# Kernel optimization log

Hardware: AMD Instinct MI355X
Metric: run time of the kernel (lower is better)

Reference implementation:

```python
import jax, jax.numpy as jnp
import numpy as np

N, E, B, L, D, H = 50000, 800000, 64, 32, 256, 256


def setup_inputs() -> dict:
    key = jax.random.key(0)
    ks = jax.random.split(key, 20)
    s = 0.05
    inp = {
        'x': jax.random.normal(ks[0], (N, D), jnp.float32),
        'edge_index': jax.random.randint(ks[1], (2, E), 0, N),
        'batch': jnp.sort(jax.random.randint(ks[2], (N,), 0, B)),
        'paths': jax.random.randint(ks[3], (B, L), 0, N),
        # SAGEConv1: lin_l (aggregated neighbors, with bias) + lin_r (root, no bias)
        'w1l': jax.random.normal(ks[4], (D, H), jnp.float32) * s,
        'b1l': jnp.zeros((H,), jnp.float32),
        'w1r': jax.random.normal(ks[5], (D, H), jnp.float32) * s,
        # SAGEConv2
        'w2l': jax.random.normal(ks[6], (H, H), jnp.float32) * s,
        'b2l': jnp.zeros((H,), jnp.float32),
        'w2r': jax.random.normal(ks[7], (H, H), jnp.float32) * s,
        # LSTM (gate order i,f,g,o as in torch)
        'w_ih': jax.random.normal(ks[8], (4 * H, H), jnp.float32) * s,
        'w_hh': jax.random.normal(ks[9], (4 * H, H), jnp.float32) * s,
        'b_ih': jnp.zeros((4 * H,), jnp.float32),
        'b_hh': jnp.zeros((4 * H,), jnp.float32),
        # scorer MLP
        'wm1': jax.random.normal(ks[10], (2 * H, H), jnp.float32) * s,
        'bm1': jnp.zeros((H,), jnp.float32),
        'wm2': jax.random.normal(ks[11], (H, 1), jnp.float32) * s,
        'bm2': jnp.zeros((1,), jnp.float32),
    }
    return inp


def sage_conv(x, src, dst, wl, bl, wr):
    # mean-aggregate neighbor features (messages flow src -> dst)
    agg = jax.ops.segment_sum(x[src], dst, num_segments=N)
    deg = jax.ops.segment_sum(jnp.ones((src.shape[0],), x.dtype), dst, num_segments=N)
    mean = agg / jnp.maximum(deg, 1.0)[:, None]
    return mean @ wl + bl + x @ wr


def lstm_last_hidden(seq, w_ih, w_hh, b_ih, b_hh):
    # seq: [B, L, H] -> hn: [B, H]
    h0 = jnp.zeros((seq.shape[0], H), seq.dtype)
    c0 = jnp.zeros_like(h0)

    def step(carry, xt):
        h, c = carry
        gates = xt @ w_ih.T + b_ih + h @ w_hh.T + b_hh
        i, f, g, o = jnp.split(gates, 4, axis=-1)
        c = jax.nn.sigmoid(f) * c + jax.nn.sigmoid(i) * jnp.tanh(g)
        h = jax.nn.sigmoid(o) * jnp.tanh(c)
        return (h, c), None

    (hn, _), _ = jax.lax.scan(step, (h0, c0), jnp.swapaxes(seq, 0, 1))
    return hn


def reference(x, edge_index, batch, paths, w1l, b1l, w1r, w2l, b2l, w2r,
              w_ih, w_hh, b_ih, b_hh, wm1, bm1, wm2, bm2):
    src, dst = edge_index[0], edge_index[1]
    h = jax.nn.relu(sage_conv(x, src, dst, w1l, b1l, w1r))
    node_emb = sage_conv(h, src, dst, w2l, b2l, w2r)  # [N, H]

    # global mean pool per graph
    gsum = jax.ops.segment_sum(node_emb, batch, num_segments=B)
    gcnt = jax.ops.segment_sum(jnp.ones((N,), node_emb.dtype), batch, num_segments=B)
    graph_emb = gsum / jnp.maximum(gcnt, 1.0)[:, None]  # [B, H]

    path_seq = node_emb[paths]  # [B, L, H]
    path_emb = lstm_last_hidden(path_seq, w_ih, w_hh, b_ih, b_hh)  # [B, H]

    combined = jnp.concatenate([graph_emb, path_emb], axis=-1)  # [B, 2H]
    scores = jax.nn.relu(combined @ wm1 + bm1) @ wm2 + bm2  # [B, 1]
    return scores.reshape(-1)  # torch.cat of per-path [1] scores -> [B]
```

## Files before the change

kernel.cpp:

```cpp
#include <hip/hip_runtime.h>

namespace {

constexpr int NN = 50000;
constexpr int NE = 800000;
constexpr int NB = 64;
constexpr int NL = 32;
constexpr int ND = 256;
constexpr int NSCAN = 196;
constexpr int NPOOL = (NN + 63) / 64;

typedef __attribute__((ext_vector_type(8))) short short8v;
typedef __attribute__((ext_vector_type(4))) float float4v;

#define GLD16(GP, LP) __builtin_amdgcn_global_load_lds( \
    (const __attribute__((address_space(1))) void*)(GP), \
    (__attribute__((address_space(3))) void*)(LP), 16, 0, 0)

__device__ __forceinline__ float sigf(float x){ return 1.0f/(1.0f + __expf(-x)); }

__device__ __forceinline__ ushort rne_bf16(float f){
  uint u = __float_as_uint(f);
  return (ushort)((u + 0x7FFFu + ((u >> 16) & 1u)) >> 16);
}
__device__ __forceinline__ float bf2f(ushort u){ return __uint_as_float((uint)u << 16); }

__device__ __forceinline__ void split1(float f, ushort& h, ushort& lo){
  uint u = __float_as_uint(f);
  h = (ushort)(u >> 16);
  float r = f - __uint_as_float(u & 0xFFFF0000u);
  lo = (ushort)(__float_as_uint(r) >> 16);
}

__device__ __forceinline__ void split8(float4 fa, float4 fb, uint4& h, uint4& lo){
  uint a0=__float_as_uint(fa.x), a1=__float_as_uint(fa.y), a2=__float_as_uint(fa.z), a3=__float_as_uint(fa.w);
  uint b0=__float_as_uint(fb.x), b1=__float_as_uint(fb.y), b2=__float_as_uint(fb.z), b3=__float_as_uint(fb.w);
  h.x = (a0>>16) | (a1 & 0xFFFF0000u);
  h.y = (a2>>16) | (a3 & 0xFFFF0000u);
  h.z = (b0>>16) | (b1 & 0xFFFF0000u);
  h.w = (b2>>16) | (b3 & 0xFFFF0000u);
  float r0 = fa.x - __uint_as_float(a0 & 0xFFFF0000u);
  float r1 = fa.y - __uint_as_float(a1 & 0xFFFF0000u);
  float r2 = fa.z - __uint_as_float(a2 & 0xFFFF0000u);
  float r3 = fa.w - __uint_as_float(a3 & 0xFFFF0000u);
  float r4 = fb.x - __uint_as_float(b0 & 0xFFFF0000u);
  float r5 = fb.y - __uint_as_float(b1 & 0xFFFF0000u);
  float r6 = fb.z - __uint_as_float(b2 & 0xFFFF0000u);
  float r7 = fb.w - __uint_as_float(b3 & 0xFFFF0000u);
  lo.x = (__float_as_uint(r0)>>16) | (__float_as_uint(r1) & 0xFFFF0000u);
  lo.y = (__float_as_uint(r2)>>16) | (__float_as_uint(r3) & 0xFFFF0000u);
  lo.z = (__float_as_uint(r4)>>16) | (__float_as_uint(r5) & 0xFFFF0000u);
  lo.w = (__float_as_uint(r6)>>16) | (__float_as_uint(r7) & 0xFFFF0000u);
}

__global__ void k_hist(const int* __restrict__ dst, int* __restrict__ cnt){
  int stride = gridDim.x * blockDim.x;
  for (int e = blockIdx.x*blockDim.x + threadIdx.x; e < NE; e += stride)
    atomicAdd(&cnt[dst[e]], 1);
}

__global__ void k_scan_block(const int* __restrict__ cnt, int* __restrict__ offs,
                             int* __restrict__ bsum){
  __shared__ int s[256];
  const int t = threadIdx.x, i = blockIdx.x*256 + t;
  int v = cnt[i];
  s[t] = v; __syncthreads();
  #pragma unroll
  for (int off = 1; off < 256; off <<= 1){
    int x = (t >= off) ? s[t-off] : 0;
    __syncthreads();
    s[t] += x;
    __syncthreads();
  }
  offs[i] = s[t] - v;
  if (t == 255) bsum[blockIdx.x] = s[255];
}

__global__ void k_scan_top(const int* __restrict__ bsum, int* __restrict__ bsum2){
  __shared__ int s[256];
  const int t = threadIdx.x;
  int v = (t < NSCAN) ? bsum[t] : 0;
  s[t] = v; __syncthreads();
  #pragma unroll
  for (int off = 1; off < 256; off <<= 1){
    int x = (t >= off) ? s[t-off] : 0;
    __syncthreads();
    s[t] += x;
    __syncthreads();
  }
  if (t < NSCAN) bsum2[t] = s[t] - v;
}

__global__ void k_scan_add(int* __restrict__ offs, const int* __restrict__ bsum2,
                           int* __restrict__ cursor){
  const int i = blockIdx.x*256 + threadIdx.x;
  int v = offs[i] + bsum2[blockIdx.x];
  offs[i] = v;
  cursor[i] = v;
}

__global__ void k_fill(const int* __restrict__ src, const int* __restrict__ dst,
                       int* __restrict__ cursor, int* __restrict__ csr){
  int stride = gridDim.x * blockDim.x;
  for (int e = blockIdx.x*blockDim.x + threadIdx.x; e < NE; e += stride){
    int d = dst[e];
    int pos = atomicAdd(&cursor[d], 1);
    csr[pos] = src[e];
  }
}

__global__ void k_tobf16(const float* __restrict__ in, ushort* __restrict__ out){
  const int i = blockIdx.x*blockDim.x + threadIdx.x;
  const float4 a = ((const float4*)in)[i*2];
  const float4 b = ((const float4*)in)[i*2+1];
  ushort o[8] = { rne_bf16(a.x), rne_bf16(a.y), rne_bf16(a.z), rne_bf16(a.w),
                  rne_bf16(b.x), rne_bf16(b.y), rne_bf16(b.z), rne_bf16(b.w) };
  ((uint4*)out)[i] = *(uint4*)o;
}

__launch_bounds__(256, 8)
__global__ void k_gather_bf16(const ushort* __restrict__ feat, const int* __restrict__ offs,
                              const int* __restrict__ csr,
                              ushort* __restrict__ outH, ushort* __restrict__ outL){
  __shared__ float4 sp[256];
  const int u = blockIdx.x, t = threadIdx.x;
  const int w = t >> 6, l = t & 63;
  const int beg = offs[u], end = offs[u+1];
  const int lc = l * 4;
  float a0 = 0.f, a1 = 0.f, a2 = 0.f, a3 = 0.f;
  int e = beg + w;
  for (; e + 4 < end; e += 8){
    int s0 = csr[e], s1 = csr[e+4];
    ushort4 v0 = *(const ushort4*)(feat + (long long)s0*ND + lc);
    ushort4 v1 = *(const ushort4*)(feat + (long long)s1*ND + lc);
    a0 += bf2f(v0.x) + bf2f(v1.x);
    a1 += bf2f(v0.y) + bf2f(v1.y);
    a2 += bf2f(v0.z) + bf2f(v1.z);
    a3 += bf2f(v0.w) + bf2f(v1.w);
  }
  if (e < end){
    int s0 = csr[e];
    ushort4 v0 = *(const ushort4*)(feat + (long long)s0*ND + lc);
    a0 += bf2f(v0.x); a1 += bf2f(v0.y); a2 += bf2f(v0.z); a3 += bf2f(v0.w);
  }
  sp[t] = make_float4(a0, a1, a2, a3);
  __syncthreads();
  if (t < 64){
    float4 p0 = sp[t], p1 = sp[64+t], p2 = sp[128+t], p3 = sp[192+t];
    float inv = 1.0f / fmaxf((float)(end - beg), 1.0f);
    float4 r;
    r.x = (p0.x + p1.x + p2.x + p3.x) * inv;
    r.y = (p0.y + p1.y + p2.y + p3.y) * inv;
    r.z = (p0.z + p1.z + p2.z + p3.z) * inv;
    r.w = (p0.w + p1.w + p2.w + p3.w) * inv;
    ushort hh[4], ll[4];
    split1(r.x, hh[0], ll[0]);
    split1(r.y, hh[1], ll[1]);
    split1(r.z, hh[2], ll[2]);
    split1(r.w, hh[3], ll[3]);
    *(ushort4*)(outH + (long long)u*ND + t*4) = *(ushort4*)hh;
    *(ushort4*)(outL + (long long)u*ND + t*4) = *(ushort4*)ll;
  }
}

__global__ void k_wsplit(const float* __restrict__ wl, const float* __restrict__ wr,
                         ushort* __restrict__ WtH, ushort* __restrict__ WtL){
  const int k = blockIdx.x;
  const int n = threadIdx.x;
  float v = (k < 256) ? wl[k*256 + n] : wr[(k-256)*256 + n];
  uint u = __float_as_uint(v);
  float r = v - __uint_as_float(u & 0xFFFF0000u);
  const int wc = n >> 6, nt = (n >> 4) & 3, lm = n & 15;
  const int kk = k >> 5, lq = (k >> 3) & 3, j = k & 7;
  const long long idx = (long long)(((wc*4 + nt)*16 + kk)*64 + lq*16 + lm)*8 + j;
  WtH[idx] = (ushort)(u >> 16);
  WtL[idx] = (ushort)(__float_as_uint(r) >> 16);
}

__launch_bounds__(256, 3)
__global__ void k_gemm_mfma(const ushort* __restrict__ A1H, const ushort* __restrict__ A1L,
                            const ushort* __restrict__ A2H, const ushort* __restrict__ A2L,
                            const float* __restrict__ A2F,
                            const ushort* __restrict__ WtH, const ushort* __restrict__ WtL,
                            const float* __restrict__ bias,
                            ushort* __restrict__ CH, ushort* __restrict__ CL,
                            ushort* __restrict__ Cb, int relu, int a2f32)
{
  __shared__ float eb[16*260];
  char* const sm = (char*)eb;

  const int t  = threadIdx.x;
  const int w  = t >> 6;
  const int l  = t & 63;
  const int lm = l & 15;
  const int lq = l >> 4;
  const int m0 = blockIdx.x * 64;

  const uint4* BH4 = (const uint4*)WtH;
  const uint4* BL4 = (const uint4*)WtL;

  const float4v vzero = {0.f, 0.f, 0.f, 0.f};
  float4v acc[4][4];
  #pragma unroll
  for (int i = 0; i < 4; ++i)
    #pragma unroll
    for (int j = 0; j < 4; ++j) acc[i][j] = vzero;

  int bbase[4];
  #pragma unroll
  for (int nt = 0; nt < 4; ++nt) bbase[nt] = (w*4 + nt)*1024 + l;

  const int j0 = w * 2;

  auto stageHL = [&](int bb, const ushort* __restrict__ H, const ushort* __restrict__ L, int k0){
    #pragma unroll
    for (int jj = 0; jj < 2; ++jj){
      const int j   = j0 + jj;
      const int arr = j >> 2;
      const int i   = j & 3;
      const int row = i*16 + (l >> 2);
      int rg = m0 + row; rg = (rg < NN) ? rg : (NN - 1);
      const int g = (l & 3) ^ ((row >> 1) & 3);
      const ushort* srcp = (arr ? L : H) + (long long)rg*ND + k0 + g*8;
      GLD16(srcp, sm + bb + arr*4096 + i*1024);
    }
  };
  auto stageF = [&](int bb, int k0){
    #pragma unroll
    for (int jj = 0; jj < 2; ++jj){
      const int j   = j0 + jj;
      const int row = j*8 + (l >> 3);
      int rg = m0 + row; rg = (rg < NN) ? rg : (NN - 1);
      const int g = (l & 7) ^ (row & 7);
      const float* srcp = A2F + (long long)rg*ND + k0 + g*4;
      GLD16(srcp, sm + bb + j*1024);
    }
  };
  auto stage = [&](int bb, int kk){
    if (kk < 8)      stageHL(bb, A1H, A1L, kk*32);
    else if (!a2f32) stageHL(bb, A2H, A2L, (kk - 8)*32);
    else             stageF (bb, (kk - 8)*32);
  };

  stage(0, 0);
  __syncthreads();

  #pragma unroll
  for (int kk = 0; kk < 16; ++kk){
    const int bb = (kk & 1) * 8192;

    uint4 bh[4], bl[4];
    #pragma unroll
    for (int nt = 0; nt < 4; ++nt){
      const int idx = bbase[nt] + kk*64;
      bh[nt] = BH4[idx];
      bl[nt] = BL4[idx];
    }

    if (kk < 15) stage(bb ^ 8192, kk + 1);

    uint4 ah[4], al[4];
    if (kk < 8 || !a2f32){
      #pragma unroll
      for (int mt = 0; mt < 4; ++mt){
        const int row = mt*16 + lm;
        const int off = bb + row*64 + ((lq ^ ((row >> 1) & 3)) << 4);
        ah[mt] = *(const uint4*)(sm + off);
        al[mt] = *(const uint4*)(sm + 4096 + off);
      }
    } else {
      #pragma unroll
      for (int mt = 0; mt < 4; ++mt){
        const int row = mt*16 + lm;
        const int s = row & 7;
        const float4 fa = *(const float4*)(sm + bb + row*128 + (((2*lq    ) ^ s) << 4));
        const float4 fb = *(const float4*)(sm + bb + row*128 + (((2*lq + 1) ^ s) << 4));
        split8(fa, fb, ah[mt], al[mt]);
      }
    }

    #pragma unroll
    for (int nt = 0; nt < 4; ++nt){
      short8v bhv = *(short8v*)&bh[nt];
      short8v blv = *(short8v*)&bl[nt];
      #pragma unroll
      for (int mt = 0; mt < 4; ++mt){
        short8v ahv = *(short8v*)&ah[mt];
        short8v alv = *(short8v*)&al[mt];
        acc[mt][nt] = __builtin_amdgcn_mfma_f32_16x16x32_bf16(ahv, bhv, acc[mt][nt], 0, 0, 0);
        acc[mt][nt] = __builtin_amdgcn_mfma_f32_16x16x32_bf16(alv, bhv, acc[mt][nt], 0, 0, 0);
        acc[mt][nt] = __builtin_amdgcn_mfma_f32_16x16x32_bf16(ahv, blv, acc[mt][nt], 0, 0, 0);
      }
    }
    __syncthreads();
  }

  float bvv[4];
  #pragma unroll
  for (int nt = 0; nt < 4; ++nt) bvv[nt] = bias[w*64 + nt*16 + lm];

  #pragma unroll
  for (int mt = 0; mt < 4; ++mt){
    #pragma unroll
    for (int nt = 0; nt < 4; ++nt){
      #pragma unroll
      for (int r = 0; r < 4; ++r){
        float v = acc[mt][nt][r] + bvv[nt];
        if (relu) v = fmaxf(v, 0.f);
        eb[(lq*4 + r)*260 + w*64 + nt*16 + lm] = v;
      }
    }
    __syncthreads();
    #pragma unroll
    for (int i = 0; i < 4; ++i){
      int idx = i*256 + t;
      int rr  = idx >> 6;
      int c4  = (idx & 63) * 4;
      int grow = m0 + mt*16 + rr;
      if (grow < NN){
        float4 fv = *(float4*)&eb[rr*260 + c4];
        ushort hh[4], ll[4];
        split1(fv.x, hh[0], ll[0]);
        split1(fv.y, hh[1], ll[1]);
        split1(fv.z, hh[2], ll[2]);
        split1(fv.w, hh[3], ll[3]);
        *(ushort4*)(CH + (long long)grow*ND + c4) = *(ushort4*)hh;
        *(ushort4*)(CL + (long long)grow*ND + c4) = *(ushort4*)ll;
        if (Cb){
          ushort ub[4] = { rne_bf16(fv.x), rne_bf16(fv.y), rne_bf16(fv.z), rne_bf16(fv.w) };
          *(ushort4*)(Cb + (long long)grow*ND + c4) = *(ushort4*)ub;
        }
      }
    }
    __syncthreads();
  }
}

__launch_bounds__(256, 3)
__global__ void k_xgate(const ushort* __restrict__ EH, const ushort* __restrict__ EL,
                        const int* __restrict__ paths,
                        const float* __restrict__ w_ih, const float* __restrict__ b_ih,
                        const float* __restrict__ b_hh, float* __restrict__ xg)
{
  __shared__ float As[16][68];
  __shared__ float Ws[16][260];
  const int t  = threadIdx.x;
  const int m0 = blockIdx.x * 64;
  const int g0 = blockIdx.y * 256;
  const int rg = t >> 5, cg = t & 31;
  const int sm = t >> 2, sj = (t & 3) * 4;

  float acc[8][8];
  #pragma unroll
  for (int i = 0; i < 8; ++i)
    #pragma unroll
    for (int j = 0; j < 8; ++j) acc[i][j] = 0.f;

  const int node = paths[m0 + sm];
  const ushort* ehrow = EH + (long long)node*ND;
  const ushort* elrow = EL + (long long)node*ND;
  const float* wrow = w_ih + (long long)(g0 + t)*ND;

  for (int k0 = 0; k0 < 256; k0 += 16){
    ushort4 hv = *(const ushort4*)(ehrow + k0 + sj);
    ushort4 lv = *(const ushort4*)(elrow + k0 + sj);
    float av0 = bf2f(hv.x) + bf2f(lv.x);
    float av1 = bf2f(hv.y) + bf2f(lv.y);
    float av2 = bf2f(hv.z) + bf2f(lv.z);
    float av3 = bf2f(hv.w) + bf2f(lv.w);
    float4 q0 = *(const float4*)(wrow + k0 + 0);
    float4 q1 = *(const float4*)(wrow + k0 + 4);
    float4 q2 = *(const float4*)(wrow + k0 + 8);
    float4 q3 = *(const float4*)(wrow + k0 + 12);
    __syncthreads();
    As[sj+0][sm]=av0; As[sj+1][sm]=av1; As[sj+2][sm]=av2; As[sj+3][sm]=av3;
    Ws[ 0][t]=q0.x; Ws[ 1][t]=q0.y; Ws[ 2][t]=q0.z; Ws[ 3][t]=q0.w;
    Ws[ 4][t]=q1.x; Ws[ 5][t]=q1.y; Ws[ 6][t]=q1.z; Ws[ 7][t]=q1.w;
    Ws[ 8][t]=q2.x; Ws[ 9][t]=q2.y; Ws[10][t]=q2.z; Ws[11][t]=q2.w;
    Ws[12][t]=q3.x; Ws[13][t]=q3.y; Ws[14][t]=q3.z; Ws[15][t]=q3.w;
    __syncthreads();
    #pragma unroll
    for (int k = 0; k < 16; ++k){
      float a[8], b[8];
      *(float4*)&a[0] = *(const float4*)&As[k][rg*8];
      *(float4*)&a[4] = *(const float4*)&As[k][rg*8+4];
      *(float4*)&b[0] = *(const float4*)&Ws[k][cg*8];
      *(float4*)&b[4] = *(const float4*)&Ws[k][cg*8+4];
      #pragma unroll
      for (int i = 0; i < 8; ++i)
        #pragma unroll
        for (int j = 0; j < 8; ++j)
          acc[i][j] = fmaf(a[i], b[j], acc[i][j]);
    }
  }

  float bv[8];
  #pragma unroll
  for (int j = 0; j < 8; ++j){ int g = g0 + cg*8 + j; bv[j] = b_ih[g] + b_hh[g]; }
  #pragma unroll
  for (int i = 0; i < 8; ++i){
    int row = m0 + rg*8 + i;
    float o[8];
    #pragma unroll
    for (int j = 0; j < 8; ++j) o[j] = acc[i][j] + bv[j];
    *(float4*)(xg + (long long)row*1024 + g0 + cg*8 + 0) = *(float4*)&o[0];
    *(float4*)(xg + (long long)row*1024 + g0 + cg*8 + 4) = *(float4*)&o[4];
  }
}

__launch_bounds__(256, 4)
__global__ void k_lstm_step(const float* __restrict__ h_in, float* __restrict__ h_out,
                            float* __restrict__ c_state, const float* __restrict__ xg,
                            const float* __restrict__ w_hh, int tstep)
{
  __shared__ float ws[4*256];
  __shared__ float hs[32*260];
  __shared__ float part[2*128];
  __shared__ float gs[128];
  const int t  = threadIdx.x;
  const int u  = blockIdx.x >> 1;
  const int b0 = (blockIdx.x & 1) * 32;

  {
    int gate = t >> 6, c4 = (t & 63) * 4;
    float4 v = *(const float4*)(w_hh + (long long)(gate*256 + u)*256 + c4);
    *(float4*)&ws[gate*256 + c4] = v;
  }
  #pragma unroll
  for (int i = 0; i < 8; ++i){
    int idx = i*256 + t;
    int b = idx >> 6, c4 = (idx & 63) * 4;
    float4 v = *(const float4*)(h_in + (long long)(b0 + b)*256 + c4);
    *(float4*)&hs[b*260 + c4] = v;
  }
  __syncthreads();

  const int b  = t & 31;
  const int g  = (t >> 5) & 3;
  const int kd = t >> 7;
  float s = 0.f;
  const float* hp = &hs[b*260 + kd*128];
  const float* wp = &ws[g*256 + kd*128];
  #pragma unroll
  for (int k4 = 0; k4 < 32; ++k4){
    float4 h4 = *(const float4*)(hp + k4*4);
    float4 w4 = *(const float4*)(wp + k4*4);
    s += h4.x*w4.x + h4.y*w4.y + h4.z*w4.z + h4.w*w4.w;
  }
  part[kd*128 + b*4 + g] = s;
  __syncthreads();

  if (t < 128){
    int bb = t >> 2, gg = t & 3;
    const float* xp = xg + ((long long)(b0 + bb)*NL + tstep)*1024;
    gs[t] = part[t] + part[128 + t] + xp[gg*256 + u];
  }
  __syncthreads();

  if (t < 32){
    float gi = gs[t*4+0], gf = gs[t*4+1], gG = gs[t*4+2], go = gs[t*4+3];
    int bb = b0 + t;
    float c_old = c_state[bb*256 + u];
    float c_new = sigf(gf)*c_old + sigf(gi)*tanhf(gG);
    c_state[bb*256 + u] = c_new;
    h_out[bb*256 + u] = sigf(go)*tanhf(c_new);
  }
}

__launch_bounds__(256, 8)
__global__ void k_pool(const ushort* __restrict__ EH, const ushort* __restrict__ EL,
                       const int* __restrict__ batch,
                       float* __restrict__ gsum, float* __restrict__ gcnt)
{
  __shared__ int bs[64];
  __shared__ int uni;
  __shared__ float spf[8*256];
  const int t  = threadIdx.x;
  const int m0 = blockIdx.x * 64;
  const int r  = t >> 5;
  const int c  = t & 31;
  if (t == 0) uni = 1;
  if (t < 64){
    int n = m0 + t;
    bs[t] = (n < NN) ? batch[n] : -1;
  }
  __syncthreads();
  if (t < 64 && bs[t] != bs[0]) uni = 0;
  __syncthreads();

  const ushort* eh = EH + (long long)m0*ND + c*8;
  const ushort* el = EL + (long long)m0*ND + c*8;

  if (uni){
    float a[8];
    #pragma unroll
    for (int j = 0; j < 8; ++j) a[j] = 0.f;
    #pragma unroll
    for (int i = 0; i < 8; ++i){
      const int row = r*8 + i;
      const uint4 hv = *(const uint4*)(eh + (long long)row*ND);
      const uint4 lv = *(const uint4*)(el + (long long)row*ND);
      const ushort* hp = (const ushort*)&hv;
      const ushort* lp = (const ushort*)&lv;
      #pragma unroll
      for (int j = 0; j < 8; ++j) a[j] += bf2f(hp[j]) + bf2f(lp[j]);
    }
    #pragma unroll
    for (int j = 0; j < 8; ++j) spf[r*256 + c*8 + j] = a[j];
    __syncthreads();
    float s = spf[t] + spf[256+t] + spf[512+t] + spf[768+t]
            + spf[1024+t] + spf[1280+t] + spf[1536+t] + spf[1792+t];
    const int g = bs[0];
    unsafeAtomicAdd(&gsum[g*256 + t], s);
    if (t == 0) unsafeAtomicAdd(&gcnt[g], 64.0f);
  } else {
    float a[8];
    #pragma unroll
    for (int j = 0; j < 8; ++j) a[j] = 0.f;
    int cur = -1, cnt = 0;
    #pragma unroll
    for (int i = 0; i < 8; ++i){
      const int row = r*8 + i;
      const int g = bs[row];
      if (g != cur){
        if (cur >= 0){
          #pragma unroll
          for (int j = 0; j < 8; ++j) unsafeAtomicAdd(&gsum[cur*256 + c*8 + j], a[j]);
          if (c == 0) unsafeAtomicAdd(&gcnt[cur], (float)cnt);
        }
        #pragma unroll
        for (int j = 0; j < 8; ++j) a[j] = 0.f;
        cnt = 0; cur = g;
      }
      if (g >= 0){
        const uint4 hv = *(const uint4*)(eh + (long long)row*ND);
        const uint4 lv = *(const uint4*)(el + (long long)row*ND);
        const ushort* hp = (const ushort*)&hv;
        const ushort* lp = (const ushort*)&lv;
        #pragma unroll
        for (int j = 0; j < 8; ++j) a[j] += bf2f(hp[j]) + bf2f(lp[j]);
        ++cnt;
      }
    }
    if (cur >= 0){
      #pragma unroll
      for (int j = 0; j < 8; ++j) unsafeAtomicAdd(&gsum[cur*256 + c*8 + j], a[j]);
      if (c == 0) unsafeAtomicAdd(&gcnt[cur], (float)cnt);
    }
  }
}

__global__ void k_score(const float* __restrict__ gsum, const float* __restrict__ gcnt,
                        const float* __restrict__ hfin, const float* __restrict__ wm1,
                        const float* __restrict__ bm1, const float* __restrict__ wm2,
                        const float* __restrict__ bm2, float* __restrict__ out)
{
  __shared__ float cs[512];
  __shared__ float red[4];
  const int b = blockIdx.x, t = threadIdx.x;
  float inv = 1.0f / fmaxf(gcnt[b], 1.0f);
  cs[t]       = gsum[b*256 + t] * inv;
  cs[256 + t] = hfin[b*256 + t];
  __syncthreads();
  float v = 0.f;
  #pragma unroll 4
  for (int k = 0; k < 512; ++k) v = fmaf(cs[k], wm1[(long long)k*256 + t], v);
  v = fmaxf(v + bm1[t], 0.f) * wm2[t];
  #pragma unroll
  for (int off = 32; off > 0; off >>= 1) v += __shfl_down(v, off, 64);
  if ((t & 63) == 0) red[t >> 6] = v;
  __syncthreads();
  if (t == 0) out[b] = red[0] + red[1] + red[2] + red[3] + bm2[0];
}

}

extern "C" void kernel_launch(void* const* d_in, const int* in_sizes, int n_in,
                              void* d_out, int out_size, void* d_ws, size_t ws_size,
                              hipStream_t stream)
{
  const float* x     = (const float*)d_in[0];
  const int*   eidx  = (const int*)  d_in[1];
  const int*   batch = (const int*)  d_in[2];
  const int*   paths = (const int*)  d_in[3];
  const float* w1l   = (const float*)d_in[4];
  const float* b1l   = (const float*)d_in[5];
  const float* w1r   = (const float*)d_in[6];
  const float* w2l   = (const float*)d_in[7];
  const float* b2l   = (const float*)d_in[8];
  const float* w2r   = (const float*)d_in[9];
  const float* w_ih  = (const float*)d_in[10];
  const float* w_hh  = (const float*)d_in[11];
  const float* b_ih  = (const float*)d_in[12];
  const float* b_hh  = (const float*)d_in[13];
  const float* wm1   = (const float*)d_in[14];
  const float* bm1   = (const float*)d_in[15];
  const float* wm2   = (const float*)d_in[16];
  const float* bm2   = (const float*)d_in[17];

  const int* src = eidx;
  const int* dst = eidx + NE;

  float* w    = (float*)d_ws;
  float* bufA = w;
  float* bufB = bufA + (long long)NN*ND;
  float* xg   = bufB + (long long)NN*ND;
  float* gsum = xg   + 2048*1024;
  float* gcnt = gsum + NB*ND;
  float* h0   = gcnt + 64;
  float* c0   = h0   + NB*ND;
  float* h1   = c0   + NB*ND;
  ushort* wt1H = (ushort*)(h1 + NB*ND);
  ushort* wt1L = wt1H + 256*512;
  ushort* wt2H = wt1L + 256*512;
  ushort* wt2L = wt2H + 256*512;
  ushort* fb16 = wt2L + 256*512;

  ushort* A1H = (ushort*)bufA;
  ushort* A1L = A1H + (long long)NN*ND;
  ushort* h1H = (ushort*)bufB;
  ushort* h1L = h1H + (long long)NN*ND;

  int* cnt    = (int*)xg;
  int* offs   = cnt    + 50432;
  int* cursor = offs   + 50432;
  int* bsum   = cursor + 50432;
  int* bsum2  = bsum   + 256;
  int* csr    = bsum2  + 256;

  k_wsplit<<<512, 256, 0, stream>>>(w1l, w1r, wt1H, wt1L);
  k_wsplit<<<512, 256, 0, stream>>>(w2l, w2r, wt2H, wt2L);

  k_tobf16<<<(NN*ND/8 + 255)/256, 256, 0, stream>>>(x, fb16);

  hipMemsetAsync(cnt, 0, 50432*sizeof(int), stream);
  k_hist<<<1024, 256, 0, stream>>>(dst, cnt);
  k_scan_block<<<NSCAN, 256, 0, stream>>>(cnt, offs, bsum);
  k_scan_top<<<1, 256, 0, stream>>>(bsum, bsum2);
  k_scan_add<<<NSCAN, 256, 0, stream>>>(offs, bsum2, cursor);
  k_fill<<<1024, 256, 0, stream>>>(src, dst, cursor, csr);

  k_gather_bf16<<<NN, 256, 0, stream>>>(fb16, offs, csr, A1H, A1L);
  k_gemm_mfma<<<(NN+63)/64, 256, 0, stream>>>(A1H, A1L, nullptr, nullptr, x,
                                              wt1H, wt1L, b1l, h1H, h1L, fb16, 1, 1);

  k_gather_bf16<<<NN, 256, 0, stream>>>(fb16, offs, csr, A1H, A1L);
  k_gemm_mfma<<<(NN+63)/64, 256, 0, stream>>>(A1H, A1L, h1H, h1L, nullptr,
                                              wt2H, wt2L, b2l, h1H, h1L, (ushort*)nullptr, 0, 0);

  hipMemsetAsync(gsum, 0, (NB*ND + 64)*sizeof(float), stream);
  k_pool<<<NPOOL, 256, 0, stream>>>(h1H, h1L, batch, gsum, gcnt);

  k_xgate<<<dim3((NB*NL)/64, 1024/256), 256, 0, stream>>>(h1H, h1L, paths, w_ih, b_ih, b_hh, xg);

  hipMemsetAsync(h0, 0, 2*(size_t)NB*ND*sizeof(float), stream);
  for (int ts = 0; ts < NL; ++ts){
    float* hin  = (ts & 1) ? h1 : h0;
    float* hout = (ts & 1) ? h0 : h1;
    k_lstm_step<<<512, 256, 0, stream>>>(hin, hout, c0, xg, w_hh, ts);
  }

  k_score<<<NB, 256, 0, stream>>>(gsum, gcnt, h0, wm1, bm1, wm2, bm2, (float*)d_out);
}
```

Baseline: 786.0 us.

## Split GEMM into per-layer kernels with register-prefetched A loads, drop LDS staging

The single GEMM kernel is replaced by two specialised kernels. Both drop LDS staging via global_load_lds and instead double-buffer A (and, for layer 2, B) tiles directly in registers, with no barrier in the k-loop. Layer 1 is split across two N-halves to launch more blocks, and it no longer writes a separate bf16 copy of h1. Instead, the layer-2 gather reads the hi part of the split, which is now rounded to nearest, so the extra output stream goes away. The cost is higher register pressure and uncoalesced direct global loads of A rows.

```diff
diff --git a/kernel.cpp b/kernel.cpp
--- a/kernel.cpp
+++ b/kernel.cpp
@@ -13,10 +13,6 @@
 typedef __attribute__((ext_vector_type(8))) short short8v;
 typedef __attribute__((ext_vector_type(4))) float float4v;
 
-#define GLD16(GP, LP) __builtin_amdgcn_global_load_lds( \
-    (const __attribute__((address_space(1))) void*)(GP), \
-    (__attribute__((address_space(3))) void*)(LP), 16, 0, 0)
-
 __device__ __forceinline__ float sigf(float x){ return 1.0f/(1.0f + __expf(-x)); }
 
 __device__ __forceinline__ ushort rne_bf16(float f){
@@ -25,10 +21,9 @@
 }
 __device__ __forceinline__ float bf2f(ushort u){ return __uint_as_float((uint)u << 16); }
 
-__device__ __forceinline__ void split1(float f, ushort& h, ushort& lo){
-  uint u = __float_as_uint(f);
-  h = (ushort)(u >> 16);
-  float r = f - __uint_as_float(u & 0xFFFF0000u);
+__device__ __forceinline__ void splitr(float f, ushort& h, ushort& lo){
+  h = rne_bf16(f);
+  float r = f - bf2f(h);
   lo = (ushort)(__float_as_uint(r) >> 16);
 }
 
@@ -154,10 +149,10 @@
     r.z = (p0.z + p1.z + p2.z + p3.z) * inv;
     r.w = (p0.w + p1.w + p2.w + p3.w) * inv;
     ushort hh[4], ll[4];
-    split1(r.x, hh[0], ll[0]);
-    split1(r.y, hh[1], ll[1]);
-    split1(r.z, hh[2], ll[2]);
-    split1(r.w, hh[3], ll[3]);
+    splitr(r.x, hh[0], ll[0]);
+    splitr(r.y, hh[1], ll[1]);
+    splitr(r.z, hh[2], ll[2]);
+    splitr(r.w, hh[3], ll[3]);
     *(ushort4*)(outH + (long long)u*ND + t*4) = *(ushort4*)hh;
     *(ushort4*)(outL + (long long)u*ND + t*4) = *(ushort4*)ll;
   }
@@ -178,121 +173,210 @@
 }
 
 __launch_bounds__(256, 3)
-__global__ void k_gemm_mfma(const ushort* __restrict__ A1H, const ushort* __restrict__ A1L,
-                            const ushort* __restrict__ A2H, const ushort* __restrict__ A2L,
-                            const float* __restrict__ A2F,
-                            const ushort* __restrict__ WtH, const ushort* __restrict__ WtL,
-                            const float* __restrict__ bias,
-                            ushort* __restrict__ CH, ushort* __restrict__ CL,
-                            ushort* __restrict__ Cb, int relu, int a2f32)
+__global__ void k_gemm_l1(const ushort* __restrict__ A1H, const ushort* __restrict__ A1L,
+                          const float* __restrict__ A2F,
+                          const ushort* __restrict__ WtH, const ushort* __restrict__ WtL,
+                          const float* __restrict__ bias,
+                          ushort* __restrict__ CH, ushort* __restrict__ CL)
 {
-  __shared__ float eb[16*260];
-  char* const sm = (char*)eb;
-
+  __shared__ float eb[16*132];
   const int t  = threadIdx.x;
   const int w  = t >> 6;
   const int l  = t & 63;
   const int lm = l & 15;
   const int lq = l >> 4;
   const int m0 = blockIdx.x * 64;
+  const int n0 = blockIdx.y * 128;
 
   const uint4* BH4 = (const uint4*)WtH;
   const uint4* BL4 = (const uint4*)WtL;
 
   const float4v vzero = {0.f, 0.f, 0.f, 0.f};
+  float4v acc[4][2];
+  #pragma unroll
+  for (int i = 0; i < 4; ++i)
+    #pragma unroll
+    for (int j = 0; j < 2; ++j) acc[i][j] = vzero;
+
+  long long arow[4];
+  #pragma unroll
+  for (int mt = 0; mt < 4; ++mt){
+    int row = m0 + mt*16 + lm;
+    row = (row < NN) ? row : (NN - 1);
+    arow[mt] = (long long)row * ND;
+  }
+  int bbase[2];
+  #pragma unroll
+  for (int j = 0; j < 2; ++j){
+    const int ncol = n0 + w*32 + j*16;
+    bbase[j] = ((ncol >> 6)*4 + ((ncol >> 4) & 3))*1024 + l;
+  }
+
+  auto ldA = [&](int kk, uint4* ah, uint4* al){
+    if (kk < 8){
+      const int koff = kk*32 + lq*8;
+      #pragma unroll
+      for (int mt = 0; mt < 4; ++mt){
+        ah[mt] = *(const uint4*)(A1H + arow[mt] + koff);
+        al[mt] = *(const uint4*)(A1L + arow[mt] + koff);
+      }
+    } else {
+      const int koff = (kk & 7)*32 + lq*8;
+      #pragma unroll
+      for (int mt = 0; mt < 4; ++mt){
+        const float* p = A2F + arow[mt] + koff;
+        float4 fa = *(const float4*)p;
+        float4 fb = *(const float4*)(p + 4);
+        split8(fa, fb, ah[mt], al[mt]);
+      }
+    }
+  };
+
+  uint4 ahb[2][4], alb[2][4];
+  ldA(0, ahb[0], alb[0]);
+
+  #pragma unroll
+  for (int kk = 0; kk < 16; ++kk){
+    const int cur = kk & 1, nx = cur ^ 1;
+    uint4 bh[2], bl[2];
+    #pragma unroll
+    for (int j = 0; j < 2; ++j){
+      const int idx = bbase[j] + kk*64;
+      bh[j] = BH4[idx];
+      bl[j] = BL4[idx];
+    }
+    if (kk < 15) ldA(kk + 1, ahb[nx], alb[nx]);
+
+    #pragma unroll
+    for (int j = 0; j < 2; ++j){
+      short8v bhv = *(short8v*)&bh[j];
+      short8v blv = *(short8v*)&bl[j];
+      #pragma unroll
+      for (int mt = 0; mt < 4; ++mt){
+        short8v ahv = *(short8v*)&ahb[cur][mt];
+        short8v alv = *(short8v*)&alb[cur][mt];
+        acc[mt][j] = __builtin_amdgcn_mfma_f32_16x16x32_bf16(ahv, bhv, acc[mt][j], 0, 0, 0);
+        acc[mt][j] = __builtin_amdgcn_mfma_f32_16x16x32_bf16(alv, bhv, acc[mt][j], 0, 0, 0);
+        acc[mt][j] = __builtin_amdgcn_mfma_f32_16x16x32_bf16(ahv, blv, acc[mt][j], 0, 0, 0);
+      }
+    }
+  }
+
+  float bvv[2];
+  #pragma unroll
+  for (int j = 0; j < 2; ++j) bvv[j] = bias[n0 + w*32 + j*16 + lm];
+
+  #pragma unroll
+  for (int mt = 0; mt < 4; ++mt){
+    #pragma unroll
+    for (int j = 0; j < 2; ++j){
+      #pragma unroll
+      for (int r = 0; r < 4; ++r){
+        float v = fmaxf(acc[mt][j][r] + bvv[j], 0.f);
+        eb[(lq*4 + r)*132 + w*32 + j*16 + lm] = v;
+      }
+    }
+    __syncthreads();
+    #pragma unroll
+    for (int i = 0; i < 2; ++i){
+      int idx = i*256 + t;
+      int rr  = idx >> 5;
+      int c4  = (idx & 31) * 4;
+      int grow = m0 + mt*16 + rr;
+      if (grow < NN){
+        float4 fv = *(float4*)&eb[rr*132 + c4];
+        ushort hh[4], ll[4];
+        splitr(fv.x, hh[0], ll[0]);
+        splitr(fv.y, hh[1], ll[1]);
+        splitr(fv.z, hh[2], ll[2]);
+        splitr(fv.w, hh[3], ll[3]);
+        *(ushort4*)(CH + (long long)grow*ND + n0 + c4) = *(ushort4*)hh;
+        *(ushort4*)(CL + (long long)grow*ND + n0 + c4) = *(ushort4*)ll;
+      }
+    }
+    __syncthreads();
+  }
+}
+
+__launch_bounds__(256, 2)
+__global__ void k_gemm_l2(const ushort* A1H, const ushort* A1L,
+                          const ushort* A2H, const ushort* A2L,
+                          const ushort* __restrict__ WtH, const ushort* __restrict__ WtL,
+                          const float* __restrict__ bias,
+                          ushort* CH, ushort* CL)
+{
+  __shared__ float eb[16*260];
+  const int t  = threadIdx.x;
+  const int w  = t >> 6;
+  const int l  = t & 63;
+  const int lm = l & 15;
+  const int lq = l >> 4;
+  const int m0 = blockIdx.x * 64;
+
+  const uint4* BH4 = (const uint4*)WtH;
+  const uint4* BL4 = (const uint4*)WtL;
+
+  const float4v vzero = {0.f, 0.f, 0.f, 0.f};
   float4v acc[4][4];
   #pragma unroll
   for (int i = 0; i < 4; ++i)
     #pragma unroll
     for (int j = 0; j < 4; ++j) acc[i][j] = vzero;
 
+  long long arow[4];
+  #pragma unroll
+  for (int mt = 0; mt < 4; ++mt){
+    int row = m0 + mt*16 + lm;
+    row = (row < NN) ? row : (NN - 1);
+    arow[mt] = (long long)row * ND;
+  }
   int bbase[4];
   #pragma unroll
   for (int nt = 0; nt < 4; ++nt) bbase[nt] = (w*4 + nt)*1024 + l;
 
-  const int j0 = w * 2;
-
-  auto stageHL = [&](int bb, const ushort* __restrict__ H, const ushort* __restrict__ L, int k0){
-    #pragma unroll
-    for (int jj = 0; jj < 2; ++jj){
-      const int j   = j0 + jj;
-      const int arr = j >> 2;
-      const int i   = j & 3;
-      const int row = i*16 + (l >> 2);
-      int rg = m0 + row; rg = (rg < NN) ? rg : (NN - 1);
-      const int g = (l & 3) ^ ((row >> 1) & 3);
-      const ushort* srcp = (arr ? L : H) + (long long)rg*ND + k0 + g*8;
-      GLD16(srcp, sm + bb + arr*4096 + i*1024);
-    }
-  };
-  auto stageF = [&](int bb, int k0){
-    #pragma unroll
-    for (int jj = 0; jj < 2; ++jj){
-      const int j   = j0 + jj;
-      const int row = j*8 + (l >> 3);
-      int rg = m0 + row; rg = (rg < NN) ? rg : (NN - 1);
-      const int g = (l & 7) ^ (row & 7);
-      const float* srcp = A2F + (long long)rg*ND + k0 + g*4;
-      GLD16(srcp, sm + bb + j*1024);
-    }
-  };
-  auto stage = [&](int bb, int kk){
-    if (kk < 8)      stageHL(bb, A1H, A1L, kk*32);
-    else if (!a2f32) stageHL(bb, A2H, A2L, (kk - 8)*32);
-    else             stageF (bb, (kk - 8)*32);
-  };
-
-  stage(0, 0);
-  __syncthreads();
-
-  #pragma unroll
-  for (int kk = 0; kk < 16; ++kk){
-    const int bb = (kk & 1) * 8192;
-
-    uint4 bh[4], bl[4];
+  auto ldB = [&](int kk, uint4* bh, uint4* bl){
     #pragma unroll
     for (int nt = 0; nt < 4; ++nt){
       const int idx = bbase[nt] + kk*64;
       bh[nt] = BH4[idx];
       bl[nt] = BL4[idx];
     }
-
-    if (kk < 15) stage(bb ^ 8192, kk + 1);
-
-    uint4 ah[4], al[4];
-    if (kk < 8 || !a2f32){
+  };
+  auto ldA = [&](int kk, uint4* ah, uint4* al){
+    const ushort* Hb = (kk < 8) ? A1H : A2H;
+    const ushort* Lb = (kk < 8) ? A1L : A2L;
+    const int koff = (kk & 7)*32 + lq*8;
+    #pragma unroll
+    for (int mt = 0; mt < 4; ++mt){
+      ah[mt] = *(const uint4*)(Hb + arow[mt] + koff);
+      al[mt] = *(const uint4*)(Lb + arow[mt] + koff);
+    }
+  };
+
+  uint4 bhb[2][4], blb[2][4], ahb[2][4], alb[2][4];
+  ldB(0, bhb[0], blb[0]);
+  ldA(0, ahb[0], alb[0]);
+
+  #pragma unroll
+  for (int kk = 0; kk < 16; ++kk){
+    const int cur = kk & 1, nx = cur ^ 1;
+    if (kk < 15){
+      ldB(kk + 1, bhb[nx], blb[nx]);
+      ldA(kk + 1, ahb[nx], alb[nx]);
+    }
+    #pragma unroll
+    for (int nt = 0; nt < 4; ++nt){
+      short8v bhv = *(short8v*)&bhb[cur][nt];
+      short8v blv = *(short8v*)&blb[cur][nt];
       #pragma unroll
       for (int mt = 0; mt < 4; ++mt){
-        const int row = mt*16 + lm;
-        const int off = bb + row*64 + ((lq ^ ((row >> 1) & 3)) << 4);
-        ah[mt] = *(const uint4*)(sm + off);
-        al[mt] = *(const uint4*)(sm + 4096 + off);
-      }
-    } else {
-      #pragma unroll
-      for (int mt = 0; mt < 4; ++mt){
-        const int row = mt*16 + lm;
-        const int s = row & 7;
-        const float4 fa = *(const float4*)(sm + bb + row*128 + (((2*lq    ) ^ s) << 4));
-        const float4 fb = *(const float4*)(sm + bb + row*128 + (((2*lq + 1) ^ s) << 4));
-        split8(fa, fb, ah[mt], al[mt]);
-      }
-    }
-
-    #pragma unroll
-    for (int nt = 0; nt < 4; ++nt){
-      short8v bhv = *(short8v*)&bh[nt];
-      short8v blv = *(short8v*)&bl[nt];
-      #pragma unroll
-      for (int mt = 0; mt < 4; ++mt){
-        short8v ahv = *(short8v*)&ah[mt];
-        short8v alv = *(short8v*)&al[mt];
+        short8v ahv = *(short8v*)&ahb[cur][mt];
+        short8v alv = *(short8v*)&alb[cur][mt];
         acc[mt][nt] = __builtin_amdgcn_mfma_f32_16x16x32_bf16(ahv, bhv, acc[mt][nt], 0, 0, 0);
         acc[mt][nt] = __builtin_amdgcn_mfma_f32_16x16x32_bf16(alv, bhv, acc[mt][nt], 0, 0, 0);
         acc[mt][nt] = __builtin_amdgcn_mfma_f32_16x16x32_bf16(ahv, blv, acc[mt][nt], 0, 0, 0);
       }
     }
-    __syncthreads();
   }
 
   float bvv[4];
@@ -306,7 +390,6 @@
       #pragma unroll
       for (int r = 0; r < 4; ++r){
         float v = acc[mt][nt][r] + bvv[nt];
-        if (relu) v = fmaxf(v, 0.f);
         eb[(lq*4 + r)*260 + w*64 + nt*16 + lm] = v;
       }
     }
@@ -320,16 +403,12 @@
       if (grow < NN){
         float4 fv = *(float4*)&eb[rr*260 + c4];
         ushort hh[4], ll[4];
-        split1(fv.x, hh[0], ll[0]);
-        split1(fv.y, hh[1], ll[1]);
-        split1(fv.z, hh[2], ll[2]);
-        split1(fv.w, hh[3], ll[3]);
+        splitr(fv.x, hh[0], ll[0]);
+        splitr(fv.y, hh[1], ll[1]);
+        splitr(fv.z, hh[2], ll[2]);
+        splitr(fv.w, hh[3], ll[3]);
         *(ushort4*)(CH + (long long)grow*ND + c4) = *(ushort4*)hh;
         *(ushort4*)(CL + (long long)grow*ND + c4) = *(ushort4*)ll;
-        if (Cb){
-          ushort ub[4] = { rne_bf16(fv.x), rne_bf16(fv.y), rne_bf16(fv.z), rne_bf16(fv.w) };
-          *(ushort4*)(Cb + (long long)grow*ND + c4) = *(ushort4*)ub;
-        }
       }
     }
     __syncthreads();
@@ -641,12 +720,10 @@
   k_fill<<<1024, 256, 0, stream>>>(src, dst, cursor, csr);
 
   k_gather_bf16<<<NN, 256, 0, stream>>>(fb16, offs, csr, A1H, A1L);
-  k_gemm_mfma<<<(NN+63)/64, 256, 0, stream>>>(A1H, A1L, nullptr, nullptr, x,
-                                              wt1H, wt1L, b1l, h1H, h1L, fb16, 1, 1);
-
-  k_gather_bf16<<<NN, 256, 0, stream>>>(fb16, offs, csr, A1H, A1L);
-  k_gemm_mfma<<<(NN+63)/64, 256, 0, stream>>>(A1H, A1L, h1H, h1L, nullptr,
-                                              wt2H, wt2L, b2l, h1H, h1L, (ushort*)nullptr, 0, 0);
+  k_gemm_l1<<<dim3(782, 2), 256, 0, stream>>>(A1H, A1L, x, wt1H, wt1L, b1l, h1H, h1L);
+
+  k_gather_bf16<<<NN, 256, 0, stream>>>(h1H, offs, csr, A1H, A1L);
+  k_gemm_l2<<<782, 256, 0, stream>>>(A1H, A1L, h1H, h1L, wt2H, wt2L, b2l, h1H, h1L);
 
   hipMemsetAsync(gsum, 0, (NB*ND + 64)*sizeof(float), stream);
   k_pool<<<NPOOL, 256, 0, stream>>>(h1H, h1L, batch, gsum, gcnt);
```

Measured after the change: 884.8 us. 12.6% more time.

## Load GEMM A tiles directly to registers with triple buffering, drop LDS staging

Applied to the files above, without the earlier changes.

The MFMA GEMM no longer stages A tiles through LDS with global_load_lds and per-iteration barriers. Each lane now loads its A fragments straight into registers with a 3-deep rotating buffer and double-buffered B loads, and the kernel is templated on the f32/relu flags. The split now rounds the high part to nearest, so that high half can feed the second-layer gather directly, which removes the separate bf16 copy write. The cost is higher register pressure (launch bounds lowered to 2 blocks) and uncoalesced direct global loads of A rows without LDS reuse.

```diff
diff --git a/kernel.cpp b/kernel.cpp
--- a/kernel.cpp
+++ b/kernel.cpp
@@ -13,10 +13,6 @@
 typedef __attribute__((ext_vector_type(8))) short short8v;
 typedef __attribute__((ext_vector_type(4))) float float4v;
 
-#define GLD16(GP, LP) __builtin_amdgcn_global_load_lds( \
-    (const __attribute__((address_space(1))) void*)(GP), \
-    (__attribute__((address_space(3))) void*)(LP), 16, 0, 0)
-
 __device__ __forceinline__ float sigf(float x){ return 1.0f/(1.0f + __expf(-x)); }
 
 __device__ __forceinline__ ushort rne_bf16(float f){
@@ -25,10 +21,9 @@
 }
 __device__ __forceinline__ float bf2f(ushort u){ return __uint_as_float((uint)u << 16); }
 
-__device__ __forceinline__ void split1(float f, ushort& h, ushort& lo){
-  uint u = __float_as_uint(f);
-  h = (ushort)(u >> 16);
-  float r = f - __uint_as_float(u & 0xFFFF0000u);
+__device__ __forceinline__ void splitr(float f, ushort& h, ushort& lo){
+  h = rne_bf16(f);
+  float r = f - bf2f(h);
   lo = (ushort)(__float_as_uint(r) >> 16);
 }
 
@@ -154,10 +149,10 @@
     r.z = (p0.z + p1.z + p2.z + p3.z) * inv;
     r.w = (p0.w + p1.w + p2.w + p3.w) * inv;
     ushort hh[4], ll[4];
-    split1(r.x, hh[0], ll[0]);
-    split1(r.y, hh[1], ll[1]);
-    split1(r.z, hh[2], ll[2]);
-    split1(r.w, hh[3], ll[3]);
+    splitr(r.x, hh[0], ll[0]);
+    splitr(r.y, hh[1], ll[1]);
+    splitr(r.z, hh[2], ll[2]);
+    splitr(r.w, hh[3], ll[3]);
     *(ushort4*)(outH + (long long)u*ND + t*4) = *(ushort4*)hh;
     *(ushort4*)(outL + (long long)u*ND + t*4) = *(ushort4*)ll;
   }
@@ -177,18 +172,16 @@
   WtL[idx] = (ushort)(__float_as_uint(r) >> 16);
 }
 
-__launch_bounds__(256, 3)
-__global__ void k_gemm_mfma(const ushort* __restrict__ A1H, const ushort* __restrict__ A1L,
-                            const ushort* __restrict__ A2H, const ushort* __restrict__ A2L,
-                            const float* __restrict__ A2F,
-                            const ushort* __restrict__ WtH, const ushort* __restrict__ WtL,
-                            const float* __restrict__ bias,
-                            ushort* __restrict__ CH, ushort* __restrict__ CL,
-                            ushort* __restrict__ Cb, int relu, int a2f32)
+template<int A2F32, int RELU>
+__launch_bounds__(256, 2)
+__global__ void k_gemm(const ushort* A1H, const ushort* A1L,
+                       const ushort* A2H, const ushort* A2L,
+                       const float*  A2F,
+                       const ushort* __restrict__ WtH, const ushort* __restrict__ WtL,
+                       const float* __restrict__ bias,
+                       ushort* CH, ushort* CL)
 {
   __shared__ float eb[16*260];
-  char* const sm = (char*)eb;
-
   const int t  = threadIdx.x;
   const int w  = t >> 6;
   const int l  = t & 63;
@@ -206,83 +199,77 @@
     #pragma unroll
     for (int j = 0; j < 4; ++j) acc[i][j] = vzero;
 
+  long long arow[4];
+  #pragma unroll
+  for (int mt = 0; mt < 4; ++mt){
+    int row = m0 + mt*16 + lm;
+    row = (row < NN) ? row : (NN - 1);
+    arow[mt] = (long long)row * ND;
+  }
   int bbase[4];
   #pragma unroll
   for (int nt = 0; nt < 4; ++nt) bbase[nt] = (w*4 + nt)*1024 + l;
 
-  const int j0 = w * 2;
-
-  auto stageHL = [&](int bb, const ushort* __restrict__ H, const ushort* __restrict__ L, int k0){
-    #pragma unroll
-    for (int jj = 0; jj < 2; ++jj){
-      const int j   = j0 + jj;
-      const int arr = j >> 2;
-      const int i   = j & 3;
-      const int row = i*16 + (l >> 2);
-      int rg = m0 + row; rg = (rg < NN) ? rg : (NN - 1);
-      const int g = (l & 3) ^ ((row >> 1) & 3);
-      const ushort* srcp = (arr ? L : H) + (long long)rg*ND + k0 + g*8;
-      GLD16(srcp, sm + bb + arr*4096 + i*1024);
-    }
-  };
-  auto stageF = [&](int bb, int k0){
-    #pragma unroll
-    for (int jj = 0; jj < 2; ++jj){
-      const int j   = j0 + jj;
-      const int row = j*8 + (l >> 3);
-      int rg = m0 + row; rg = (rg < NN) ? rg : (NN - 1);
-      const int g = (l & 7) ^ (row & 7);
-      const float* srcp = A2F + (long long)rg*ND + k0 + g*4;
-      GLD16(srcp, sm + bb + j*1024);
-    }
-  };
-  auto stage = [&](int bb, int kk){
-    if (kk < 8)      stageHL(bb, A1H, A1L, kk*32);
-    else if (!a2f32) stageHL(bb, A2H, A2L, (kk - 8)*32);
-    else             stageF (bb, (kk - 8)*32);
-  };
-
-  stage(0, 0);
-  __syncthreads();
-
-  #pragma unroll
-  for (int kk = 0; kk < 16; ++kk){
-    const int bb = (kk & 1) * 8192;
-
-    uint4 bh[4], bl[4];
+  uint4 aP[3][4], aQ[3][4];
+  uint4 bh[2][4], bl[2][4];
+
+  auto ldB = [&](int kk, int s){
     #pragma unroll
     for (int nt = 0; nt < 4; ++nt){
       const int idx = bbase[nt] + kk*64;
-      bh[nt] = BH4[idx];
-      bl[nt] = BL4[idx];
-    }
-
-    if (kk < 15) stage(bb ^ 8192, kk + 1);
+      bh[s][nt] = BH4[idx];
+      bl[s][nt] = BL4[idx];
+    }
+  };
+  auto ldA = [&](int kk, int s){
+    const int koff = (kk & 7)*32 + lq*8;
+    if (kk < 8 || !A2F32){
+      const ushort* Hb = (kk < 8) ? A1H : A2H;
+      const ushort* Lb = (kk < 8) ? A1L : A2L;
+      #pragma unroll
+      for (int mt = 0; mt < 4; ++mt){
+        aP[s][mt] = *(const uint4*)(Hb + arow[mt] + koff);
+        aQ[s][mt] = *(const uint4*)(Lb + arow[mt] + koff);
+      }
+    } else {
+      #pragma unroll
+      for (int mt = 0; mt < 4; ++mt){
+        const float* p = A2F + arow[mt] + koff;
+        aP[s][mt] = *(const uint4*)p;
+        aQ[s][mt] = *(const uint4*)(p + 4);
+      }
+    }
+  };
+
+  ldA(0, 0);
+  ldB(0, 0);
+  ldA(1, 1);
+
+  #pragma unroll
+  for (int kk = 0; kk < 16; ++kk){
+    const int c3 = kk % 3;
+    const int cB = kk & 1;
+    if (kk < 15) ldB(kk + 1, cB ^ 1);
+    if (kk < 14) ldA(kk + 2, (kk + 2) % 3);
+    __builtin_amdgcn_sched_barrier(0);
 
     uint4 ah[4], al[4];
-    if (kk < 8 || !a2f32){
+    if (kk < 8 || !A2F32){
+      #pragma unroll
+      for (int mt = 0; mt < 4; ++mt){ ah[mt] = aP[c3][mt]; al[mt] = aQ[c3][mt]; }
+    } else {
       #pragma unroll
       for (int mt = 0; mt < 4; ++mt){
-        const int row = mt*16 + lm;
-        const int off = bb + row*64 + ((lq ^ ((row >> 1) & 3)) << 4);
-        ah[mt] = *(const uint4*)(sm + off);
-        al[mt] = *(const uint4*)(sm + 4096 + off);
-      }
-    } else {
-      #pragma unroll
-      for (int mt = 0; mt < 4; ++mt){
-        const int row = mt*16 + lm;
-        const int s = row & 7;
-        const float4 fa = *(const float4*)(sm + bb + row*128 + (((2*lq    ) ^ s) << 4));
-        const float4 fb = *(const float4*)(sm + bb + row*128 + (((2*lq + 1) ^ s) << 4));
+        float4 fa = *(float4*)&aP[c3][mt];
+        float4 fb = *(float4*)&aQ[c3][mt];
         split8(fa, fb, ah[mt], al[mt]);
       }
     }
 
     #pragma unroll
     for (int nt = 0; nt < 4; ++nt){
-      short8v bhv = *(short8v*)&bh[nt];
-      short8v blv = *(short8v*)&bl[nt];
+      short8v bhv = *(short8v*)&bh[cB][nt];
+      short8v blv = *(short8v*)&bl[cB][nt];
       #pragma unroll
       for (int mt = 0; mt < 4; ++mt){
         short8v ahv = *(short8v*)&ah[mt];
@@ -292,7 +279,6 @@
         acc[mt][nt] = __builtin_amdgcn_mfma_f32_16x16x32_bf16(ahv, blv, acc[mt][nt], 0, 0, 0);
       }
     }
-    __syncthreads();
   }
 
   float bvv[4];
@@ -306,7 +292,7 @@
       #pragma unroll
       for (int r = 0; r < 4; ++r){
         float v = acc[mt][nt][r] + bvv[nt];
-        if (relu) v = fmaxf(v, 0.f);
+        if (RELU) v = fmaxf(v, 0.f);
         eb[(lq*4 + r)*260 + w*64 + nt*16 + lm] = v;
       }
     }
@@ -320,16 +306,12 @@
       if (grow < NN){
         float4 fv = *(float4*)&eb[rr*260 + c4];
         ushort hh[4], ll[4];
-        split1(fv.x, hh[0], ll[0]);
-        split1(fv.y, hh[1], ll[1]);
-        split1(fv.z, hh[2], ll[2]);
-        split1(fv.w, hh[3], ll[3]);
+        splitr(fv.x, hh[0], ll[0]);
+        splitr(fv.y, hh[1], ll[1]);
+        splitr(fv.z, hh[2], ll[2]);
+        splitr(fv.w, hh[3], ll[3]);
         *(ushort4*)(CH + (long long)grow*ND + c4) = *(ushort4*)hh;
         *(ushort4*)(CL + (long long)grow*ND + c4) = *(ushort4*)ll;
-        if (Cb){
-          ushort ub[4] = { rne_bf16(fv.x), rne_bf16(fv.y), rne_bf16(fv.z), rne_bf16(fv.w) };
-          *(ushort4*)(Cb + (long long)grow*ND + c4) = *(ushort4*)ub;
-        }
       }
     }
     __syncthreads();
@@ -641,12 +623,12 @@
   k_fill<<<1024, 256, 0, stream>>>(src, dst, cursor, csr);
 
   k_gather_bf16<<<NN, 256, 0, stream>>>(fb16, offs, csr, A1H, A1L);
-  k_gemm_mfma<<<(NN+63)/64, 256, 0, stream>>>(A1H, A1L, nullptr, nullptr, x,
-                                              wt1H, wt1L, b1l, h1H, h1L, fb16, 1, 1);
-
-  k_gather_bf16<<<NN, 256, 0, stream>>>(fb16, offs, csr, A1H, A1L);
-  k_gemm_mfma<<<(NN+63)/64, 256, 0, stream>>>(A1H, A1L, h1H, h1L, nullptr,
-                                              wt2H, wt2L, b2l, h1H, h1L, (ushort*)nullptr, 0, 0);
+  k_gemm<1,1><<<782, 256, 0, stream>>>(A1H, A1L, nullptr, nullptr, x,
+                                       wt1H, wt1L, b1l, h1H, h1L);
+
+  k_gather_bf16<<<NN, 256, 0, stream>>>(h1H, offs, csr, A1H, A1L);
+  k_gemm<0,0><<<782, 256, 0, stream>>>(A1H, A1L, h1H, h1L, nullptr,
+                                       wt2H, wt2L, b2l, h1H, h1L);
 
   hipMemsetAsync(gsum, 0, (NB*ND + 64)*sizeof(float), stream);
   k_pool<<<NPOOL, 256, 0, stream>>>(h1H, h1L, batch, gsum, gcnt);
```

Result: slower. 816.6 us (+3.9%).
